# Kernel tuning notes

Hardware: AMD Instinct MI355X
Metric: run time of the kernel (lower is better)

## Reference

```python
import jax, jax.numpy as jnp
import numpy as np

N_NODES = 100000
N_EDGES = 3200000
NUM_CLASSES = 10
SQRT3 = 3.0 ** 0.5


def setup_inputs() -> dict:
    key = jax.random.key(0)
    ks = jax.random.split(key, 20)
    f32 = jnp.float32
    return {
        "positions": jax.random.normal(ks[0], (N_NODES, 3), f32) * 5.0,
        "edge_src": jax.random.randint(ks[1], (N_EDGES,), 0, N_NODES, jnp.int32),
        "edge_dst": jax.random.randint(ks[2], (N_EDGES,), 0, N_NODES, jnp.int32),
        # layer1: TP('1x0e', sh) -> '1x0e + 1x1o' -> Linear -> '5x0e + 5x1o'
        "W0_1": jax.random.normal(ks[3], (5, 1), f32),
        "W1_1": jax.random.normal(ks[4], (5, 1, 3), f32),
        "b_1": jax.random.normal(ks[5], (5,), f32),
        # gate1: Linear('5x0e+5x1o' -> '10x0e') uses only the 5 input 0e irreps
        "Wg1": jax.random.normal(ks[6], (10, 5), f32),
        "bg1": jax.random.normal(ks[7], (10,), f32),
        # layer2: TP('5x0e+5x1o', sh) -> 10x0e + 10x1o (+5x1e unused) -> '5x0e+5x1o'
        "W0_2": jax.random.normal(ks[8], (5, 10), f32),
        "W1_2": jax.random.normal(ks[9], (5, 10, 3), f32),
        "b_2": jax.random.normal(ks[10], (5,), f32),
        "Wg2": jax.random.normal(ks[11], (10, 5), f32),
        "bg2": jax.random.normal(ks[12], (10,), f32),
        # layer3: TP -> 10x0e used -> '5x0e'
        "W0_3": jax.random.normal(ks[13], (5, 10), f32),
        "b_3": jax.random.normal(ks[14], (5,), f32),
        "Wg3": jax.random.normal(ks[15], (10, 5), f32),
        "bg3": jax.random.normal(ks[16], (10,), f32),
        "Wout": jax.random.normal(ks[17], (NUM_CLASSES, 5), f32) * 0.3,
        "bout": jax.random.normal(ks[18], (NUM_CLASSES,), f32) * 0.1,
    }


def _sh1(rel):
    # component-normalized real spherical harmonics, lmax=1: Y0 = 1, Y1 = sqrt(3)*r_hat
    r = jnp.linalg.norm(rel, axis=-1, keepdims=True)
    return SQRT3 * rel / jnp.maximum(r, 1e-9)  # [E,3]


def _scatter_mean(x, dst, n):
    s = jax.ops.segment_sum(x, dst, num_segments=n)
    cnt = jax.ops.segment_sum(jnp.ones((x.shape[0],), x.dtype), dst, num_segments=n)
    cnt = jnp.maximum(cnt, 1.0).reshape((n,) + (1,) * (x.ndim - 1))
    return s / cnt


def _layer(s, v, sh1, dst, n, W0, b, W1=None):
    # per-edge CG tensor product of dest-node features with edge SH, then linear, then scatter-mean
    sd = s[dst]                                            # [E,a0] gather 0e feats
    tp_s = [sd]                                            # 0e x 0e(Y0=1) -> 0e
    if v is not None:
        vd = v[dst]                                        # [E,a1,3] gather 1o feats
        tp_s.append(jnp.einsum('eic,ec->ei', vd, sh1) / SQRT3)  # 1o x 1o -> 0e (CG dot)
    tp_s = jnp.concatenate(tp_s, axis=1)
    out_s = _scatter_mean(tp_s @ W0.T + b, dst, n)         # [N,out0]
    if W1 is None:
        return out_s, None
    tp_v = [sd[:, :, None] * sh1[:, None, :]]              # 0e x 1o -> 1o
    if v is not None:
        tp_v.append(vd)                                    # 1o x 0e(Y0=1) -> 1o
    tp_v = jnp.concatenate(tp_v, axis=1)                   # [E,in1,3]
    out_v = _scatter_mean(jnp.einsum('eic,oic->eoc', tp_v, W1), dst, n)
    return out_s, out_v


def _gate(s, v, Wg, bg):
    # ActivationLayer: gate each irrep by GELU of a learned scalar (torch GELU = exact erf)
    g = jax.nn.gelu(s @ Wg.T + bg, approximate=False)
    n0 = s.shape[1]
    gs = g[:, :n0] * s
    if v is None:
        return gs, None
    return gs, g[:, n0:n0 + v.shape[1], None] * v


def reference(positions, edge_src, edge_dst, W0_1, W1_1, b_1, Wg1, bg1,
              W0_2, W1_2, b_2, Wg2, bg2, W0_3, b_3, Wg3, bg3, Wout, bout):
    n = positions.shape[0]
    rel = positions[edge_dst] - positions[edge_src]
    sh1 = _sh1(rel)
    s = jnp.ones((n, 1), positions.dtype)  # dummy '1x0e' starting node features
    s, v = _layer(s, None, sh1, edge_dst, n, W0_1, b_1, W1_1)
    s, v = _gate(s, v, Wg1, bg1)
    s, v = _layer(s, v, sh1, edge_dst, n, W0_2, b_2, W1_2)
    s, v = _gate(s, v, Wg2, bg2)
    s, _ = _layer(s, v, sh1, edge_dst, n, W0_3, b_3, None)
    s, _ = _gate(s, None, Wg3, bg3)
    pooled = jnp.mean(s, axis=0)                       # avg over nodes -> [5]
    return jax.nn.softmax(pooled @ Wout.T + bout)      # [NUM_CLASSES]
```

## Files before the change

kernel.cpp:

```cpp
#include <hip/hip_runtime.h>
#include <math.h>

#define SQRT3F 1.7320508075688772f
#define INV_SQRT3F 0.57735026918962576f
typedef unsigned long long u64;
typedef unsigned int u32;

#define PK_SCALE 1024.0f
#define PK_BIAS  2048u
#define PK_MASK  0x7FFFFull

#define NPR     4096
#define NRANGE  25
#define OVF_CAP 131072

__device__ __forceinline__ float gelu_exact(float x) {
    return 0.5f * x * (1.0f + erff(x * 0.70710678118654752f));
}

__device__ __forceinline__ u64 make_rec4(const float4* __restrict__ pos4, int s, int d) {
    float4 pd = pos4[d];
    float4 ps = pos4[s];
    float rx = pd.x - ps.x;
    float ry = pd.y - ps.y;
    float rz = pd.z - ps.z;
    float rr = sqrtf(rx*rx + ry*ry + rz*rz);
    float inv = (SQRT3F * 16384.0f) / fmaxf(rr, 1e-9f);
    u32 ax = (u32)__float2int_rn(rx * inv) + 32768u;
    u32 ay = (u32)__float2int_rn(ry * inv) + 32768u;
    u32 az = (u32)__float2int_rn(rz * inv) + 32768u;
    return ((u64)ax << 44) | ((u64)ay << 28) | ((u64)az << 12) | (u64)(d & (NPR - 1));
}

__device__ __forceinline__ u64 rec_to_w(u64 rec) {
    u32 az = (u32)((rec >> 12) & 0xFFFF);
    u32 ay = (u32)((rec >> 28) & 0xFFFF);
    u32 ax = (u32)((rec >> 44) & 0xFFFF);
    return (u64)((ax + 8u) >> 4) | ((u64)((ay + 8u) >> 4) << 19)
         | ((u64)((az + 8u) >> 4) << 38) | (1ull << 57);
}

__global__ __launch_bounds__(256) void pack_pos_kernel(
    const float* __restrict__ pos, float4* __restrict__ pos4, int N)
{
    int i = blockIdx.x * 256 + threadIdx.x;
    if (i < N) pos4[i] = make_float4(pos[3*i], pos[3*i+1], pos[3*i+2], 0.f);
}

__global__ __launch_bounds__(1024, 8) void scatter_kernel(
    const float4* __restrict__ pos4,
    const int* __restrict__ src,
    const int* __restrict__ dst,
    u64* __restrict__ buckets, u32* __restrict__ cnts,
    u64* __restrict__ ovf_rec, u32* __restrict__ ovf_node, u64* __restrict__ ovf_cnt,
    int E, int span, int CAP)
{
    __shared__ u32 scnt[NRANGE];
    const int p = blockIdx.x;
    if (threadIdx.x < NRANGE) scnt[threadIdx.x] = 0;
    __syncthreads();

    const int start = p * span;
    int end = start + span;
    if (end > E) end = E;
    u64* const bkt = buckets + (size_t)p * NRANGE * (size_t)CAP;

    for (int i0 = start + (int)threadIdx.x * 4; i0 < end; i0 += 1024 * 4) {
        if (i0 + 4 <= end) {
            int4 da = *reinterpret_cast<const int4*>(dst + i0);
            int4 sa = *reinterpret_cast<const int4*>(src + i0);
            int d[4], s[4];
            d[0]=da.x; d[1]=da.y; d[2]=da.z; d[3]=da.w;
            s[0]=sa.x; s[1]=sa.y; s[2]=sa.z; s[3]=sa.w;
            u64 rec[4]; int r[4];
            #pragma unroll
            for (int k = 0; k < 4; ++k) {
                rec[k] = make_rec4(pos4, s[k], d[k]);
                r[k] = d[k] >> 12;
            }
            u32 slot[4];
            #pragma unroll
            for (int k = 0; k < 4; ++k) slot[k] = atomicAdd(&scnt[r[k]], 1u);
            #pragma unroll
            for (int k = 0; k < 4; ++k) {
                if (slot[k] < (u32)CAP) {
                    bkt[(size_t)r[k] * CAP + slot[k]] = rec[k];
                } else {
                    u64 os = atomicAdd(ovf_cnt, 1ull);
                    if (os < OVF_CAP) { ovf_rec[os] = rec[k]; ovf_node[os] = (u32)d[k]; }
                }
            }
        } else {
            for (int i = i0; i < end; ++i) {
                int dd = dst[i], ss = src[i];
                u64 rec = make_rec4(pos4, ss, dd);
                int r = dd >> 12;
                u32 slot = atomicAdd(&scnt[r], 1u);
                if (slot < (u32)CAP) bkt[(size_t)r * CAP + slot] = rec;
                else {
                    u64 os = atomicAdd(ovf_cnt, 1ull);
                    if (os < OVF_CAP) { ovf_rec[os] = rec; ovf_node[os] = (u32)dd; }
                }
            }
        }
    }
    __syncthreads();
    if (threadIdx.x < NRANGE) {
        u32 c = scnt[threadIdx.x];
        cnts[p * NRANGE + threadIdx.x] = c < (u32)CAP ? c : (u32)CAP;
    }
}

__global__ __launch_bounds__(512) void gather_kernel(
    const u64* __restrict__ buckets, const u32* __restrict__ cnts,
    const u64* __restrict__ ovf_rec, const u32* __restrict__ ovf_node,
    const u64* __restrict__ ovf_cnt,
    u64* __restrict__ reps, int P, int CAP, int R2)
{
    __shared__ u64 bins[NPR];
    __shared__ u32 segn[64];
    const int r  = blockIdx.x % NRANGE;
    const int c2 = blockIdx.x / NRANGE;

    for (int j = threadIdx.x; j < NPR; j += 512) bins[j] = 0;
    const int nseg = (P - c2 + R2 - 1) / R2;
    if ((int)threadIdx.x < nseg)
        segn[threadIdx.x] = cnts[(c2 + (int)threadIdx.x * R2) * NRANGE + r];
    __syncthreads();

    for (int sgi = 0; sgi < nseg; ++sgi) {
        int p = c2 + sgi * R2;
        u32 n = segn[sgi];
        const u64* seg = buckets + ((size_t)p * NRANGE + r) * (size_t)CAP;
        for (u32 t2 = threadIdx.x * 2; t2 < n; t2 += 1024) {
            if (t2 + 2 <= n) {
                ulonglong2 rv = *reinterpret_cast<const ulonglong2*>(seg + t2);
                atomicAdd(&bins[(u32)(rv.x & (NPR - 1))], rec_to_w(rv.x));
                atomicAdd(&bins[(u32)(rv.y & (NPR - 1))], rec_to_w(rv.y));
            } else {
                u64 rec = seg[t2];
                atomicAdd(&bins[(u32)(rec & (NPR - 1))], rec_to_w(rec));
            }
        }
    }
    if (c2 == 0) {
        u64 n = *ovf_cnt; if (n > OVF_CAP) n = OVF_CAP;
        for (u64 t = threadIdx.x; t < n; t += 512) {
            u32 dn = ovf_node[t];
            if ((int)(dn >> 12) == r)
                atomicAdd(&bins[dn & (NPR - 1)], rec_to_w(ovf_rec[t]));
        }
    }
    __syncthreads();

    u64* outp = reps + (size_t)c2 * ((size_t)NRANGE * NPR) + (size_t)r * NPR;
    for (int j = threadIdx.x; j < NPR; j += 512) outp[j] = bins[j];
}

__global__ __launch_bounds__(256, 4) void edge_bin_kernel(
    const float* __restrict__ pos,
    const int* __restrict__ src,
    const int* __restrict__ dst,
    u64* __restrict__ reps, int E, int span)
{
    __shared__ u64 bins[NPR];
    __shared__ u32 q[4][128];
    const int g = blockIdx.x;
    const int xcd = g & 7;
    const int slot = g >> 3;
    const int c = xcd + 8 * (slot / NRANGE);
    const int r = slot % NRANGE;
    const int base = r * NPR;
    const int lane = threadIdx.x & 63;
    const int wid  = threadIdx.x >> 6;
    const u64 ltmask = (1ull << lane) - 1ull;

    for (int j = threadIdx.x; j < NPR; j += 256) bins[j] = 0;
    __syncthreads();

    const int start = c * span;
    int end = start + span;
    if (end > E) end = E;
    const int niter = (end > start) ? ((end - start + 1023) >> 10) : 0;
    int qcount = 0;

    auto process = [&](u32 i2) {
        int s2 = src[i2]; int d2 = dst[i2];
        u32 j = (u32)(d2 - base);
        float rx = pos[3*d2+0] - pos[3*s2+0];
        float ry = pos[3*d2+1] - pos[3*s2+1];
        float rz = pos[3*d2+2] - pos[3*s2+2];
        float rr = sqrtf(rx*rx + ry*ry + rz*rz);
        float inv = (SQRT3F * PK_SCALE) / fmaxf(rr, 1e-9f);
        u32 ax = (u32)__float2int_rn(rx * inv) + PK_BIAS;
        u32 ay = (u32)__float2int_rn(ry * inv) + PK_BIAS;
        u32 az = (u32)__float2int_rn(rz * inv) + PK_BIAS;
        u64 w = (u64)ax | ((u64)ay << 19) | ((u64)az << 38) | (1ull << 57);
        atomicAdd(&bins[j], w);
    };

    for (int t = 0; t < niter; ++t) {
        int i0 = start + ((int)threadIdx.x << 2) + (t << 10);
        int4 d4 = make_int4(-1, -1, -1, -1);
        if (i0 + 4 <= end) d4 = *reinterpret_cast<const int4*>(dst + i0);
        else if (i0 < end) for (int k = 0; i0 + k < end; ++k) (&d4.x)[k] = dst[i0 + k];
        #pragma unroll
        for (int k = 0; k < 4; ++k) {
            int i = i0 + k;
            bool in = (i < end) && ((u32)((&d4.x)[k] - base) < NPR);
            u64 mask = __ballot(in);
            if (in) q[wid][qcount + __popcll(mask & ltmask)] = (u32)i;
            qcount += (int)__popcll(mask);
            if (qcount >= 64) { qcount -= 64; process(q[wid][qcount + lane]); }
        }
    }
    if (lane < qcount) process(q[wid][lane]);
    __syncthreads();

    u64* outp = reps + (size_t)c * ((size_t)NRANGE * NPR) + base;
    for (int j = threadIdx.x; j < NPR; j += 256) outp[j] = bins[j];
}

__global__ __launch_bounds__(256) void node_kernel(
    const u64* __restrict__ reps, size_t repStride, int R,
    const float* __restrict__ W0_1, const float* __restrict__ W1_1, const float* __restrict__ b_1,
    const float* __restrict__ Wg1,  const float* __restrict__ bg1,
    const float* __restrict__ W0_2, const float* __restrict__ W1_2, const float* __restrict__ b_2,
    const float* __restrict__ Wg2,  const float* __restrict__ bg2,
    const float* __restrict__ W0_3, const float* __restrict__ b_3,
    const float* __restrict__ Wg3,  const float* __restrict__ bg3,
    float* __restrict__ partials, int N)
{
    int d = blockIdx.x * blockDim.x + threadIdx.x;
    float sf[5] = {0.f, 0.f, 0.f, 0.f, 0.f};

    if (d < N) {
        u64 w = 0;
        int r = 0;
        for (; r + 4 <= R; r += 4) {
            u64 a0 = reps[(size_t)(r+0) * repStride + (u32)d];
            u64 a1 = reps[(size_t)(r+1) * repStride + (u32)d];
            u64 a2 = reps[(size_t)(r+2) * repStride + (u32)d];
            u64 a3 = reps[(size_t)(r+3) * repStride + (u32)d];
            w += a0 + a1 + a2 + a3;
        }
        for (; r < R; ++r) w += reps[(size_t)r * repStride + (u32)d];
        u32 deg = (u32)(w >> 57);
        if (deg > 0) {
            long long bias = (long long)deg << 11;
            float invdS = 1.0f / (PK_SCALE * (float)deg);
            float m[3];
            m[0] = (float)((long long)( w        & PK_MASK) - bias) * invdS;
            m[1] = (float)((long long)((w >> 19) & PK_MASK) - bias) * invdS;
            m[2] = (float)((long long)((w >> 38) & PK_MASK) - bias) * invdS;

            float s1[5], v1[5][3];
            #pragma unroll
            for (int i = 0; i < 5; ++i) {
                s1[i] = W0_1[i] + b_1[i];
                #pragma unroll
                for (int c = 0; c < 3; ++c) v1[i][c] = W1_1[i*3+c] * m[c];
            }
            float g1[10];
            #pragma unroll
            for (int j = 0; j < 10; ++j) {
                float t = bg1[j];
                #pragma unroll
                for (int i = 0; i < 5; ++i) t += Wg1[j*5+i] * s1[i];
                g1[j] = gelu_exact(t);
            }
            #pragma unroll
            for (int i = 0; i < 5; ++i) {
                s1[i] *= g1[i];
                #pragma unroll
                for (int c = 0; c < 3; ++c) v1[i][c] *= g1[5+i];
            }

            float dot1[5];
            #pragma unroll
            for (int i = 0; i < 5; ++i)
                dot1[i] = (v1[i][0]*m[0] + v1[i][1]*m[1] + v1[i][2]*m[2]) * INV_SQRT3F;
            float s2[5];
            #pragma unroll
            for (int o = 0; o < 5; ++o) {
                float t = b_2[o];
                #pragma unroll
                for (int i = 0; i < 5; ++i) t += W0_2[o*10+i] * s1[i];
                #pragma unroll
                for (int i = 0; i < 5; ++i) t += W0_2[o*10+5+i] * dot1[i];
                s2[o] = t;
            }
            float v2[5][3];
            #pragma unroll
            for (int o = 0; o < 5; ++o) {
                #pragma unroll
                for (int c = 0; c < 3; ++c) {
                    float t = 0.f;
                    #pragma unroll
                    for (int i = 0; i < 5; ++i) {
                        t += W1_2[(o*10+i)*3+c]   * (s1[i] * m[c]);
                        t += W1_2[(o*10+5+i)*3+c] * v1[i][c];
                    }
                    v2[o][c] = t;
                }
            }
            float g2[10];
            #pragma unroll
            for (int j = 0; j < 10; ++j) {
                float t = bg2[j];
                #pragma unroll
                for (int i = 0; i < 5; ++i) t += Wg2[j*5+i] * s2[i];
                g2[j] = gelu_exact(t);
            }
            #pragma unroll
            for (int i = 0; i < 5; ++i) {
                s2[i] *= g2[i];
                #pragma unroll
                for (int c = 0; c < 3; ++c) v2[i][c] *= g2[5+i];
            }

            float dot2[5];
            #pragma unroll
            for (int i = 0; i < 5; ++i)
                dot2[i] = (v2[i][0]*m[0] + v2[i][1]*m[1] + v2[i][2]*m[2]) * INV_SQRT3F;
            float s3[5];
            #pragma unroll
            for (int o = 0; o < 5; ++o) {
                float t = b_3[o];
                #pragma unroll
                for (int i = 0; i < 5; ++i) t += W0_3[o*10+i] * s2[i];
                #pragma unroll
                for (int i = 0; i < 5; ++i) t += W0_3[o*10+5+i] * dot2[i];
                s3[o] = t;
            }
            #pragma unroll
            for (int i = 0; i < 5; ++i) {
                float t = bg3[i];
                #pragma unroll
                for (int j = 0; j < 5; ++j) t += Wg3[i*5+j] * s3[j];
                sf[i] = gelu_exact(t) * s3[i];
            }
        }
    }

    #pragma unroll
    for (int k = 0; k < 5; ++k) {
        float v = sf[k];
        for (int off = 32; off > 0; off >>= 1) v += __shfl_down(v, off);
        sf[k] = v;
    }
    __shared__ float lred[4][5];
    int wid = threadIdx.x >> 6, lane = threadIdx.x & 63;
    if (lane == 0) {
        #pragma unroll
        for (int k = 0; k < 5; ++k) lred[wid][k] = sf[k];
    }
    __syncthreads();
    if (threadIdx.x == 0) {
        #pragma unroll
        for (int k = 0; k < 5; ++k)
            partials[blockIdx.x * 5 + k] = lred[0][k] + lred[1][k] + lred[2][k] + lred[3][k];
    }
}

__global__ __launch_bounds__(256) void finalize_kernel(
    const float* __restrict__ partials, int nb,
    const float* __restrict__ Wout, const float* __restrict__ bout,
    float* __restrict__ out, float invN)
{
    float s[5] = {0.f, 0.f, 0.f, 0.f, 0.f};
    for (int b = threadIdx.x; b < nb; b += 256) {
        #pragma unroll
        for (int k = 0; k < 5; ++k) s[k] += partials[b * 5 + k];
    }
    #pragma unroll
    for (int k = 0; k < 5; ++k) {
        float v = s[k];
        for (int off = 32; off > 0; off >>= 1) v += __shfl_down(v, off);
        s[k] = v;
    }
    __shared__ float lred[4][5];
    int wid = threadIdx.x >> 6, lane = threadIdx.x & 63;
    if (lane == 0) {
        #pragma unroll
        for (int k = 0; k < 5; ++k) lred[wid][k] = s[k];
    }
    __syncthreads();
    if (threadIdx.x == 0) {
        float pooled[5];
        #pragma unroll
        for (int i = 0; i < 5; ++i)
            pooled[i] = (lred[0][i] + lred[1][i] + lred[2][i] + lred[3][i]) * invN;
        float lg[10], mx = -1e30f;
        #pragma unroll
        for (int j = 0; j < 10; ++j) {
            float t = bout[j];
            #pragma unroll
            for (int i = 0; i < 5; ++i) t += Wout[j*5+i] * pooled[i];
            lg[j] = t;
            mx = fmaxf(mx, t);
        }
        float se = 0.f;
        #pragma unroll
        for (int j = 0; j < 10; ++j) { lg[j] = expf(lg[j] - mx); se += lg[j]; }
        float inv = 1.0f / se;
        #pragma unroll
        for (int j = 0; j < 10; ++j) out[j] = lg[j] * inv;
    }
}

extern "C" void kernel_launch(void* const* d_in, const int* in_sizes, int n_in,
                              void* d_out, int out_size, void* d_ws, size_t ws_size,
                              hipStream_t stream) {
    const float* pos  = (const float*)d_in[0];
    const int*   esrc = (const int*)d_in[1];
    const int*   edst = (const int*)d_in[2];
    const float* W0_1 = (const float*)d_in[3];
    const float* W1_1 = (const float*)d_in[4];
    const float* b_1  = (const float*)d_in[5];
    const float* Wg1  = (const float*)d_in[6];
    const float* bg1  = (const float*)d_in[7];
    const float* W0_2 = (const float*)d_in[8];
    const float* W1_2 = (const float*)d_in[9];
    const float* b_2  = (const float*)d_in[10];
    const float* Wg2  = (const float*)d_in[11];
    const float* bg2  = (const float*)d_in[12];
    const float* W0_3 = (const float*)d_in[13];
    const float* b_3  = (const float*)d_in[14];
    const float* Wg3  = (const float*)d_in[15];
    const float* bg3  = (const float*)d_in[16];
    const float* Wout = (const float*)d_in[17];
    const float* bout = (const float*)d_in[18];

    const int N = in_sizes[0] / 3;
    const int E = in_sizes[1];
    const size_t repStride = (size_t)NRANGE * NPR;
    const int nblocks = (N + 255) / 256;

    int P = 0, CAP = 0, R2 = 0;
    size_t off_pos4 = 0, off_reps = 0, off_cnts = 0, off_ovfc = 0, off_ovfn = 0,
           off_ovfr = 0, off_bkts = 0;
    {
        const int pcand[8]  = {512, 448, 384, 320, 256, 192, 128, 64};
        const int r2cand[4] = {16, 8, 4, 2};
        for (int b = 0; b < 8 && !P; ++b) {
            for (int a = 0; a < 4; ++a) {
                int p = pcand[b];
                long span = (((long)E + p - 1) / p + 3) & ~3L;
                long mean = (span + NRANGE - 1) / NRANGE;
                long slack = mean / 4 > 128 ? mean / 4 : 128;
                long cap = (mean + slack + 7) & ~7L;
                size_t off = 16384;
                size_t o_pos4 = off; off += ((size_t)N * 16 + 255) & ~(size_t)255;
                size_t o_reps = off; off += (size_t)r2cand[a] * repStride * 8;
                size_t o_cnts = off; off += ((size_t)p * NRANGE * 4 + 255) & ~(size_t)255;
                size_t o_ovfc = off; off += 256;
                size_t o_ovfn = off; off += (size_t)OVF_CAP * 4;
                size_t o_ovfr = off; off += (size_t)OVF_CAP * 8;
                size_t o_bkts = off; off += (size_t)p * NRANGE * cap * 8;
                if (off <= ws_size) {
                    P = p; CAP = (int)cap; R2 = r2cand[a];
                    off_pos4 = o_pos4; off_reps = o_reps; off_cnts = o_cnts;
                    off_ovfc = o_ovfc; off_ovfn = o_ovfn; off_ovfr = o_ovfr;
                    off_bkts = o_bkts;
                    break;
                }
            }
        }
    }

    float* partials = (float*)d_ws;

    if (P) {
        float4* pos4  = (float4*)((char*)d_ws + off_pos4);
        u64* reps     = (u64*)((char*)d_ws + off_reps);
        u32* cnts     = (u32*)((char*)d_ws + off_cnts);
        u64* ovf_cnt  = (u64*)((char*)d_ws + off_ovfc);
        u32* ovf_node = (u32*)((char*)d_ws + off_ovfn);
        u64* ovf_rec  = (u64*)((char*)d_ws + off_ovfr);
        u64* buckets  = (u64*)((char*)d_ws + off_bkts);

        hipMemsetAsync(ovf_cnt, 0, 64, stream);
        pack_pos_kernel<<<nblocks, 256, 0, stream>>>(pos, pos4, N);
        int span = (int)((((size_t)E + P - 1) / P + 3) & ~(size_t)3);
        scatter_kernel<<<P, 1024, 0, stream>>>(pos4, esrc, edst,
            buckets, cnts, ovf_rec, ovf_node, ovf_cnt, E, span, CAP);
        gather_kernel<<<R2 * NRANGE, 512, 0, stream>>>(buckets, cnts,
            ovf_rec, ovf_node, ovf_cnt, reps, P, CAP, R2);
        node_kernel<<<nblocks, 256, 0, stream>>>(reps, repStride, R2,
            W0_1, W1_1, b_1, Wg1, bg1,
            W0_2, W1_2, b_2, Wg2, bg2,
            W0_3, b_3, Wg3, bg3,
            partials, N);
    } else {
        u64* reps = (u64*)((char*)d_ws + 16384);
        size_t avail = ws_size > 16384 ? ws_size - 16384 : 0;
        int C = (int)(avail / (repStride * 8));
        if (C > 48) C = 48;
        C &= ~7;
        if (C >= 8) {
            int span = (int)((((size_t)E + C - 1) / C + 3) & ~(size_t)3);
            edge_bin_kernel<<<NRANGE * C, 256, 0, stream>>>(pos, esrc, edst, reps, E, span);
            node_kernel<<<nblocks, 256, 0, stream>>>(reps, repStride, C,
                W0_1, W1_1, b_1, Wg1, bg1,
                W0_2, W1_2, b_2, Wg2, bg2,
                W0_3, b_3, Wg3, bg3,
                partials, N);
        }
    }

    finalize_kernel<<<1, 256, 0, stream>>>(partials, nblocks, Wout, bout,
                                           (float*)d_out, 1.0f / (float)N);
}
```

Before: 87.39 us.

## Bucket compact 32-bit edge records and compute SH in gather with LDS-cached positions

```diff
diff --git a/kernel.cpp b/kernel.cpp
--- a/kernel.cpp
+++ b/kernel.cpp
@@ -7,154 +7,152 @@
 typedef unsigned int u32;
 
 #define PK_SCALE 1024.0f
-#define PK_BIAS  2048u
 #define PK_MASK  0x7FFFFull
 
-#define NPR     4096
-#define NRANGE  25
+#define NPR2   2048
+#define NRG2   49
+#define REP2   ((size_t)NRG2 * NPR2)
+#define EPB    4096
 #define OVF_CAP 131072
+
+#define NPR    4096
+#define NRANGE 25
 
 __device__ __forceinline__ float gelu_exact(float x) {
     return 0.5f * x * (1.0f + erff(x * 0.70710678118654752f));
 }
 
-__device__ __forceinline__ u64 make_rec4(const float4* __restrict__ pos4, int s, int d) {
-    float4 pd = pos4[d];
-    float4 ps = pos4[s];
-    float rx = pd.x - ps.x;
-    float ry = pd.y - ps.y;
-    float rz = pd.z - ps.z;
+__device__ __forceinline__ u64 sh_to_w(float rx, float ry, float rz) {
     float rr = sqrtf(rx*rx + ry*ry + rz*rz);
-    float inv = (SQRT3F * 16384.0f) / fmaxf(rr, 1e-9f);
-    u32 ax = (u32)__float2int_rn(rx * inv) + 32768u;
-    u32 ay = (u32)__float2int_rn(ry * inv) + 32768u;
-    u32 az = (u32)__float2int_rn(rz * inv) + 32768u;
-    return ((u64)ax << 44) | ((u64)ay << 28) | ((u64)az << 12) | (u64)(d & (NPR - 1));
-}
-
-__device__ __forceinline__ u64 rec_to_w(u64 rec) {
-    u32 az = (u32)((rec >> 12) & 0xFFFF);
-    u32 ay = (u32)((rec >> 28) & 0xFFFF);
-    u32 ax = (u32)((rec >> 44) & 0xFFFF);
-    return (u64)((ax + 8u) >> 4) | ((u64)((ay + 8u) >> 4) << 19)
-         | ((u64)((az + 8u) >> 4) << 38) | (1ull << 57);
+    float inv = (SQRT3F * PK_SCALE) / fmaxf(rr, 1e-9f);
+    u32 ax = (u32)__float2int_rn(rx * inv) + 2048u;
+    u32 ay = (u32)__float2int_rn(ry * inv) + 2048u;
+    u32 az = (u32)__float2int_rn(rz * inv) + 2048u;
+    return (u64)ax | ((u64)ay << 19) | ((u64)az << 38) | (1ull << 57);
 }
 
 __global__ __launch_bounds__(256) void pack_pos_kernel(
-    const float* __restrict__ pos, float4* __restrict__ pos4, int N)
+    const float* __restrict__ pos, float4* __restrict__ pos4,
+    u64* __restrict__ ovf_cnt, u32* __restrict__ done, int N)
 {
     int i = blockIdx.x * 256 + threadIdx.x;
     if (i < N) pos4[i] = make_float4(pos[3*i], pos[3*i+1], pos[3*i+2], 0.f);
-}
-
-__global__ __launch_bounds__(1024, 8) void scatter_kernel(
+    if (blockIdx.x == 0 && threadIdx.x == 0) { *ovf_cnt = 0; *done = 0; }
+}
+
+__global__ __launch_bounds__(1024) void scatter_kernel(
+    const int* __restrict__ src, const int* __restrict__ dst,
+    u32* __restrict__ buckets, u32* __restrict__ cnts,
+    u32* __restrict__ ovf_rec, u32* __restrict__ ovf_node, u64* __restrict__ ovf_cnt,
+    int E, int CAP)
+{
+    __shared__ u32 scnt[NRG2];
+    const int p = blockIdx.x;
+    if (threadIdx.x < NRG2) scnt[threadIdx.x] = 0;
+    __syncthreads();
+
+    const int start = p * EPB;
+    int end = start + EPB;
+    if (end > E) end = E;
+    u32* const bkt = buckets + (size_t)p * NRG2 * (size_t)CAP;
+
+    int i0 = start + (int)threadIdx.x * 4;
+    if (i0 + 4 <= end) {
+        int4 d4 = *reinterpret_cast<const int4*>(dst + i0);
+        int4 s4 = *reinterpret_cast<const int4*>(src + i0);
+        int d[4] = {d4.x, d4.y, d4.z, d4.w};
+        int s[4] = {s4.x, s4.y, s4.z, s4.w};
+        u32 rec[4]; int r[4];
+        #pragma unroll
+        for (int k = 0; k < 4; ++k) {
+            r[k] = d[k] >> 11;
+            rec[k] = ((u32)s[k] << 11) | ((u32)d[k] & 2047u);
+        }
+        u32 slot[4];
+        #pragma unroll
+        for (int k = 0; k < 4; ++k) slot[k] = atomicAdd(&scnt[r[k]], 1u);
+        #pragma unroll
+        for (int k = 0; k < 4; ++k) {
+            if (slot[k] < (u32)CAP) {
+                bkt[(size_t)r[k] * CAP + slot[k]] = rec[k];
+            } else {
+                u64 os = atomicAdd(ovf_cnt, 1ull);
+                if (os < OVF_CAP) { ovf_rec[os] = rec[k]; ovf_node[os] = (u32)d[k]; }
+            }
+        }
+    } else if (i0 < end) {
+        for (int i = i0; i < end; ++i) {
+            int dd = dst[i], ss = src[i];
+            int r = dd >> 11;
+            u32 rec = ((u32)ss << 11) | ((u32)dd & 2047u);
+            u32 slot = atomicAdd(&scnt[r], 1u);
+            if (slot < (u32)CAP) bkt[(size_t)r * CAP + slot] = rec;
+            else {
+                u64 os = atomicAdd(ovf_cnt, 1ull);
+                if (os < OVF_CAP) { ovf_rec[os] = rec; ovf_node[os] = (u32)dd; }
+            }
+        }
+    }
+    __syncthreads();
+    if (threadIdx.x < NRG2) {
+        u32 c = scnt[threadIdx.x];
+        cnts[p * NRG2 + threadIdx.x] = c < (u32)CAP ? c : (u32)CAP;
+    }
+}
+
+__global__ __launch_bounds__(512) void gather_kernel(
     const float4* __restrict__ pos4,
-    const int* __restrict__ src,
-    const int* __restrict__ dst,
-    u64* __restrict__ buckets, u32* __restrict__ cnts,
-    u64* __restrict__ ovf_rec, u32* __restrict__ ovf_node, u64* __restrict__ ovf_cnt,
-    int E, int span, int CAP)
+    const u32* __restrict__ buckets, const u32* __restrict__ cnts,
+    const u32* __restrict__ ovf_rec, const u32* __restrict__ ovf_node,
+    const u64* __restrict__ ovf_cnt,
+    u64* __restrict__ reps, int P, int CAP, int R2, int N)
 {
-    __shared__ u32 scnt[NRANGE];
-    const int p = blockIdx.x;
-    if (threadIdx.x < NRANGE) scnt[threadIdx.x] = 0;
-    __syncthreads();
-
-    const int start = p * span;
-    int end = start + span;
-    if (end > E) end = E;
-    u64* const bkt = buckets + (size_t)p * NRANGE * (size_t)CAP;
-
-    for (int i0 = start + (int)threadIdx.x * 4; i0 < end; i0 += 1024 * 4) {
-        if (i0 + 4 <= end) {
-            int4 da = *reinterpret_cast<const int4*>(dst + i0);
-            int4 sa = *reinterpret_cast<const int4*>(src + i0);
-            int d[4], s[4];
-            d[0]=da.x; d[1]=da.y; d[2]=da.z; d[3]=da.w;
-            s[0]=sa.x; s[1]=sa.y; s[2]=sa.z; s[3]=sa.w;
-            u64 rec[4]; int r[4];
-            #pragma unroll
-            for (int k = 0; k < 4; ++k) {
-                rec[k] = make_rec4(pos4, s[k], d[k]);
-                r[k] = d[k] >> 12;
-            }
-            u32 slot[4];
-            #pragma unroll
-            for (int k = 0; k < 4; ++k) slot[k] = atomicAdd(&scnt[r[k]], 1u);
-            #pragma unroll
-            for (int k = 0; k < 4; ++k) {
-                if (slot[k] < (u32)CAP) {
-                    bkt[(size_t)r[k] * CAP + slot[k]] = rec[k];
-                } else {
-                    u64 os = atomicAdd(ovf_cnt, 1ull);
-                    if (os < OVF_CAP) { ovf_rec[os] = rec[k]; ovf_node[os] = (u32)d[k]; }
-                }
-            }
-        } else {
-            for (int i = i0; i < end; ++i) {
-                int dd = dst[i], ss = src[i];
-                u64 rec = make_rec4(pos4, ss, dd);
-                int r = dd >> 12;
-                u32 slot = atomicAdd(&scnt[r], 1u);
-                if (slot < (u32)CAP) bkt[(size_t)r * CAP + slot] = rec;
-                else {
-                    u64 os = atomicAdd(ovf_cnt, 1ull);
-                    if (os < OVF_CAP) { ovf_rec[os] = rec; ovf_node[os] = (u32)dd; }
-                }
-            }
-        }
-    }
-    __syncthreads();
-    if (threadIdx.x < NRANGE) {
-        u32 c = scnt[threadIdx.x];
-        cnts[p * NRANGE + threadIdx.x] = c < (u32)CAP ? c : (u32)CAP;
-    }
-}
-
-__global__ __launch_bounds__(512) void gather_kernel(
-    const u64* __restrict__ buckets, const u32* __restrict__ cnts,
-    const u64* __restrict__ ovf_rec, const u32* __restrict__ ovf_node,
-    const u64* __restrict__ ovf_cnt,
-    u64* __restrict__ reps, int P, int CAP, int R2)
-{
-    __shared__ u64 bins[NPR];
-    __shared__ u32 segn[64];
-    const int r  = blockIdx.x % NRANGE;
-    const int c2 = blockIdx.x / NRANGE;
-
-    for (int j = threadIdx.x; j < NPR; j += 512) bins[j] = 0;
+    __shared__ u64 bins[NPR2];
+    __shared__ float4 posl[NPR2];
+    __shared__ u32 segn[128];
+    const int r  = blockIdx.x % NRG2;
+    const int c2 = blockIdx.x / NRG2;
+    const int base = r * NPR2;
+
+    for (int j = threadIdx.x; j < NPR2; j += 512) {
+        bins[j] = 0;
+        int g = base + j;
+        posl[j] = (g < N) ? pos4[g] : make_float4(0.f, 0.f, 0.f, 0.f);
+    }
     const int nseg = (P - c2 + R2 - 1) / R2;
-    if ((int)threadIdx.x < nseg)
-        segn[threadIdx.x] = cnts[(c2 + (int)threadIdx.x * R2) * NRANGE + r];
-    __syncthreads();
-
-    for (int sgi = 0; sgi < nseg; ++sgi) {
-        int p = c2 + sgi * R2;
-        u32 n = segn[sgi];
-        const u64* seg = buckets + ((size_t)p * NRANGE + r) * (size_t)CAP;
-        for (u32 t2 = threadIdx.x * 2; t2 < n; t2 += 1024) {
-            if (t2 + 2 <= n) {
-                ulonglong2 rv = *reinterpret_cast<const ulonglong2*>(seg + t2);
-                atomicAdd(&bins[(u32)(rv.x & (NPR - 1))], rec_to_w(rv.x));
-                atomicAdd(&bins[(u32)(rv.y & (NPR - 1))], rec_to_w(rv.y));
-            } else {
-                u64 rec = seg[t2];
-                atomicAdd(&bins[(u32)(rec & (NPR - 1))], rec_to_w(rec));
-            }
+    for (int t = threadIdx.x; t < nseg; t += 512)
+        segn[t] = cnts[(c2 + t * R2) * NRG2 + r];
+    __syncthreads();
+
+    const int wid = threadIdx.x >> 6, lane = threadIdx.x & 63;
+    for (int sgi = wid; sgi < nseg; sgi += 8) {
+        const int p = c2 + sgi * R2;
+        const u32 n = segn[sgi];
+        const u32* seg = buckets + ((size_t)p * NRG2 + r) * (size_t)CAP;
+        for (u32 t = lane; t < n; t += 64) {
+            u32 rec = seg[t];
+            u32 j = rec & 2047u, s = rec >> 11;
+            float4 ps = pos4[s];
+            float4 pd = posl[j];
+            atomicAdd(&bins[j], sh_to_w(pd.x - ps.x, pd.y - ps.y, pd.z - ps.z));
         }
     }
     if (c2 == 0) {
         u64 n = *ovf_cnt; if (n > OVF_CAP) n = OVF_CAP;
         for (u64 t = threadIdx.x; t < n; t += 512) {
-            u32 dn = ovf_node[t];
-            if ((int)(dn >> 12) == r)
-                atomicAdd(&bins[dn & (NPR - 1)], rec_to_w(ovf_rec[t]));
-        }
-    }
-    __syncthreads();
-
-    u64* outp = reps + (size_t)c2 * ((size_t)NRANGE * NPR) + (size_t)r * NPR;
-    for (int j = threadIdx.x; j < NPR; j += 512) outp[j] = bins[j];
+            u32 dd = ovf_node[t];
+            if ((int)(dd >> 11) == r) {
+                u32 rec = ovf_rec[t];
+                u32 j = rec & 2047u, s = rec >> 11;
+                float4 ps = pos4[s]; float4 pd = posl[j];
+                atomicAdd(&bins[j], sh_to_w(pd.x - ps.x, pd.y - ps.y, pd.z - ps.z));
+            }
+        }
+    }
+    __syncthreads();
+
+    u64* outp = reps + (size_t)c2 * REP2 + base;
+    for (int j = threadIdx.x; j < NPR2; j += 512) outp[j] = bins[j];
 }
 
 __global__ __launch_bounds__(256, 4) void edge_bin_kernel(
@@ -187,16 +185,9 @@
     auto process = [&](u32 i2) {
         int s2 = src[i2]; int d2 = dst[i2];
         u32 j = (u32)(d2 - base);
-        float rx = pos[3*d2+0] - pos[3*s2+0];
-        float ry = pos[3*d2+1] - pos[3*s2+1];
-        float rz = pos[3*d2+2] - pos[3*s2+2];
-        float rr = sqrtf(rx*rx + ry*ry + rz*rz);
-        float inv = (SQRT3F * PK_SCALE) / fmaxf(rr, 1e-9f);
-        u32 ax = (u32)__float2int_rn(rx * inv) + PK_BIAS;
-        u32 ay = (u32)__float2int_rn(ry * inv) + PK_BIAS;
-        u32 az = (u32)__float2int_rn(rz * inv) + PK_BIAS;
-        u64 w = (u64)ax | ((u64)ay << 19) | ((u64)az << 38) | (1ull << 57);
-        atomicAdd(&bins[j], w);
+        atomicAdd(&bins[j], sh_to_w(pos[3*d2+0]-pos[3*s2+0],
+                                    pos[3*d2+1]-pos[3*s2+1],
+                                    pos[3*d2+2]-pos[3*s2+2]));
     };
 
     for (int t = 0; t < niter; ++t) {
@@ -221,6 +212,7 @@
     for (int j = threadIdx.x; j < NPR; j += 256) outp[j] = bins[j];
 }
 
+template<bool FUSE>
 __global__ __launch_bounds__(256) void node_kernel(
     const u64* __restrict__ reps, size_t repStride, int R,
     const float* __restrict__ W0_1, const float* __restrict__ W1_1, const float* __restrict__ b_1,
@@ -229,7 +221,9 @@
     const float* __restrict__ Wg2,  const float* __restrict__ bg2,
     const float* __restrict__ W0_3, const float* __restrict__ b_3,
     const float* __restrict__ Wg3,  const float* __restrict__ bg3,
-    float* __restrict__ partials, int N)
+    float* __restrict__ partials, int N,
+    const float* __restrict__ Wout, const float* __restrict__ bout,
+    float* __restrict__ out, float invN, u32* __restrict__ done)
 {
     int d = blockIdx.x * blockDim.x + threadIdx.x;
     float sf[5] = {0.f, 0.f, 0.f, 0.f, 0.f};
@@ -350,6 +344,7 @@
         sf[k] = v;
     }
     __shared__ float lred[4][5];
+    __shared__ int islast;
     int wid = threadIdx.x >> 6, lane = threadIdx.x & 63;
     if (lane == 0) {
         #pragma unroll
@@ -360,6 +355,55 @@
         #pragma unroll
         for (int k = 0; k < 5; ++k)
             partials[blockIdx.x * 5 + k] = lred[0][k] + lred[1][k] + lred[2][k] + lred[3][k];
+    }
+
+    if (FUSE) {
+        if (threadIdx.x == 0) {
+            __threadfence();
+            u32 old = atomicAdd(done, 1u);
+            islast = (old == gridDim.x - 1);
+        }
+        __syncthreads();
+        if (!islast) return;
+        __threadfence();
+        float s[5] = {0.f, 0.f, 0.f, 0.f, 0.f};
+        for (int b = threadIdx.x; b < (int)gridDim.x; b += 256) {
+            #pragma unroll
+            for (int k = 0; k < 5; ++k) s[k] += partials[b * 5 + k];
+        }
+        #pragma unroll
+        for (int k = 0; k < 5; ++k) {
+            float v = s[k];
+            for (int off = 32; off > 0; off >>= 1) v += __shfl_down(v, off);
+            s[k] = v;
+        }
+        __syncthreads();
+        if (lane == 0) {
+            #pragma unroll
+            for (int k = 0; k < 5; ++k) lred[wid][k] = s[k];
+        }
+        __syncthreads();
+        if (threadIdx.x == 0) {
+            float pooled[5];
+            #pragma unroll
+            for (int i = 0; i < 5; ++i)
+                pooled[i] = (lred[0][i] + lred[1][i] + lred[2][i] + lred[3][i]) * invN;
+            float lg[10], mx = -1e30f;
+            #pragma unroll
+            for (int j = 0; j < 10; ++j) {
+                float t = bout[j];
+                #pragma unroll
+                for (int i = 0; i < 5; ++i) t += Wout[j*5+i] * pooled[i];
+                lg[j] = t;
+                mx = fmaxf(mx, t);
+            }
+            float se = 0.f;
+            #pragma unroll
+            for (int j = 0; j < 10; ++j) { lg[j] = expf(lg[j] - mx); se += lg[j]; }
+            float inv = 1.0f / se;
+            #pragma unroll
+            for (int j = 0; j < 10; ++j) out[j] = lg[j] * inv;
+        }
     }
 }
 
@@ -434,66 +478,55 @@
 
     const int N = in_sizes[0] / 3;
     const int E = in_sizes[1];
-    const size_t repStride = (size_t)NRANGE * NPR;
     const int nblocks = (N + 255) / 256;
-
-    int P = 0, CAP = 0, R2 = 0;
-    size_t off_pos4 = 0, off_reps = 0, off_cnts = 0, off_ovfc = 0, off_ovfn = 0,
-           off_ovfr = 0, off_bkts = 0;
+    const int P = (E + EPB - 1) / EPB;
+
     {
-        const int pcand[8]  = {512, 448, 384, 320, 256, 192, 128, 64};
-        const int r2cand[4] = {16, 8, 4, 2};
-        for (int b = 0; b < 8 && !P; ++b) {
-            for (int a = 0; a < 4; ++a) {
-                int p = pcand[b];
-                long span = (((long)E + p - 1) / p + 3) & ~3L;
-                long mean = (span + NRANGE - 1) / NRANGE;
-                long slack = mean / 4 > 128 ? mean / 4 : 128;
-                long cap = (mean + slack + 7) & ~7L;
-                size_t off = 16384;
-                size_t o_pos4 = off; off += ((size_t)N * 16 + 255) & ~(size_t)255;
-                size_t o_reps = off; off += (size_t)r2cand[a] * repStride * 8;
-                size_t o_cnts = off; off += ((size_t)p * NRANGE * 4 + 255) & ~(size_t)255;
-                size_t o_ovfc = off; off += 256;
-                size_t o_ovfn = off; off += (size_t)OVF_CAP * 4;
-                size_t o_ovfr = off; off += (size_t)OVF_CAP * 8;
-                size_t o_bkts = off; off += (size_t)p * NRANGE * cap * 8;
-                if (off <= ws_size) {
-                    P = p; CAP = (int)cap; R2 = r2cand[a];
-                    off_pos4 = o_pos4; off_reps = o_reps; off_cnts = o_cnts;
-                    off_ovfc = o_ovfc; off_ovfn = o_ovfn; off_ovfr = o_ovfr;
-                    off_bkts = o_bkts;
-                    break;
-                }
-            }
-        }
-    }
-
-    float* partials = (float*)d_ws;
-
-    if (P) {
-        float4* pos4  = (float4*)((char*)d_ws + off_pos4);
-        u64* reps     = (u64*)((char*)d_ws + off_reps);
-        u32* cnts     = (u32*)((char*)d_ws + off_cnts);
-        u64* ovf_cnt  = (u64*)((char*)d_ws + off_ovfc);
-        u32* ovf_node = (u32*)((char*)d_ws + off_ovfn);
-        u64* ovf_rec  = (u64*)((char*)d_ws + off_ovfr);
-        u64* buckets  = (u64*)((char*)d_ws + off_bkts);
-
-        hipMemsetAsync(ovf_cnt, 0, 64, stream);
-        pack_pos_kernel<<<nblocks, 256, 0, stream>>>(pos, pos4, N);
-        int span = (int)((((size_t)E + P - 1) / P + 3) & ~(size_t)3);
-        scatter_kernel<<<P, 1024, 0, stream>>>(pos4, esrc, edst,
-            buckets, cnts, ovf_rec, ovf_node, ovf_cnt, E, span, CAP);
-        gather_kernel<<<R2 * NRANGE, 512, 0, stream>>>(buckets, cnts,
-            ovf_rec, ovf_node, ovf_cnt, reps, P, CAP, R2);
-        node_kernel<<<nblocks, 256, 0, stream>>>(reps, repStride, R2,
-            W0_1, W1_1, b_1, Wg1, bg1,
-            W0_2, W1_2, b_2, Wg2, bg2,
-            W0_3, b_3, Wg3, bg3,
-            partials, N);
-    } else {
+        const int r2c[3] = {16, 8, 4};
+        int mean = (EPB + NRG2 - 1) / NRG2;
+        int slack = mean / 2 > 64 ? mean / 2 : 64;
+        int CAP = ((mean + slack + 15) / 16) * 16;
+
+        for (int a = 0; a < 3; ++a) {
+            int R2 = r2c[a];
+            size_t off = 16384;
+            size_t o_ctr  = off; off += 256;
+            size_t o_pos4 = off; off += ((size_t)N * 16 + 255) & ~(size_t)255;
+            size_t o_reps = off; off += (size_t)R2 * REP2 * 8;
+            size_t o_cnts = off; off += ((size_t)P * NRG2 * 4 + 255) & ~(size_t)255;
+            size_t o_ovfn = off; off += (size_t)OVF_CAP * 4;
+            size_t o_ovfr = off; off += (size_t)OVF_CAP * 4;
+            size_t o_bkts = off; off += (size_t)P * NRG2 * CAP * 4;
+            if (off > ws_size) continue;
+
+            float*  partials = (float*)d_ws;
+            u64*    ovf_cnt  = (u64*)((char*)d_ws + o_ctr);
+            u32*    done     = (u32*)((char*)d_ws + o_ctr + 8);
+            float4* pos4     = (float4*)((char*)d_ws + o_pos4);
+            u64*    reps     = (u64*)((char*)d_ws + o_reps);
+            u32*    cnts     = (u32*)((char*)d_ws + o_cnts);
+            u32*    ovf_node = (u32*)((char*)d_ws + o_ovfn);
+            u32*    ovf_rec  = (u32*)((char*)d_ws + o_ovfr);
+            u32*    buckets  = (u32*)((char*)d_ws + o_bkts);
+
+            pack_pos_kernel<<<nblocks, 256, 0, stream>>>(pos, pos4, ovf_cnt, done, N);
+            scatter_kernel<<<P, 1024, 0, stream>>>(esrc, edst,
+                buckets, cnts, ovf_rec, ovf_node, ovf_cnt, E, CAP);
+            gather_kernel<<<NRG2 * R2, 512, 0, stream>>>(pos4, buckets, cnts,
+                ovf_rec, ovf_node, ovf_cnt, reps, P, CAP, R2, N);
+            node_kernel<true><<<nblocks, 256, 0, stream>>>(reps, REP2, R2,
+                W0_1, W1_1, b_1, Wg1, bg1,
+                W0_2, W1_2, b_2, Wg2, bg2,
+                W0_3, b_3, Wg3, bg3,
+                partials, N, Wout, bout, (float*)d_out, 1.0f / (float)N, done);
+            return;
+        }
+    }
+
+    {
+        float* partials = (float*)d_ws;
         u64* reps = (u64*)((char*)d_ws + 16384);
+        const size_t repStride = (size_t)NRANGE * NPR;
         size_t avail = ws_size > 16384 ? ws_size - 16384 : 0;
         int C = (int)(avail / (repStride * 8));
         if (C > 48) C = 48;
@@ -501,14 +534,13 @@
         if (C >= 8) {
             int span = (int)((((size_t)E + C - 1) / C + 3) & ~(size_t)3);
             edge_bin_kernel<<<NRANGE * C, 256, 0, stream>>>(pos, esrc, edst, reps, E, span);
-            node_kernel<<<nblocks, 256, 0, stream>>>(reps, repStride, C,
+            node_kernel<false><<<nblocks, 256, 0, stream>>>(reps, repStride, C,
                 W0_1, W1_1, b_1, Wg1, bg1,
                 W0_2, W1_2, b_2, Wg2, bg2,
                 W0_3, b_3, Wg3, bg3,
-                partials, N);
-        }
-    }
-
-    finalize_kernel<<<1, 256, 0, stream>>>(partials, nblocks, Wout, bout,
-                                           (float*)d_out, 1.0f / (float)N);
-}
+                partials, N, nullptr, nullptr, nullptr, 0.f, nullptr);
+            finalize_kernel<<<1, 256, 0, stream>>>(partials, nblocks, Wout, bout,
+                                                   (float*)d_out, 1.0f / (float)N);
+        }
+    }
+}
```

Result: faster. 78.15 us (-10.6%).
